# Kernel tuning notes

Hardware: AMD Instinct MI355X
Metric: run time of the kernel (lower is better)

The kernel has to match this reference:

```python
import jax, jax.numpy as jnp
import numpy as np

DIM = 4096
N_HEADS = 32
N_KV_HEADS = 8
HEAD_DIM = DIM // N_HEADS  # 128
B, S = 1, 2048
ROPE_THETA = 10000.0


def setup_inputs() -> dict:
    key = jax.random.key(0)
    kx, kq, kk, kv, ko = jax.random.split(key, 5)
    x = jax.random.normal(kx, (B, S, DIM), dtype=jnp.float32)
    # torch Linear weights are [out_features, in_features]
    wq = jax.random.normal(kq, (N_HEADS * HEAD_DIM, DIM), dtype=jnp.float32) * 0.02
    wk = jax.random.normal(kk, (N_KV_HEADS * HEAD_DIM, DIM), dtype=jnp.float32) * 0.02
    wv = jax.random.normal(kv, (N_KV_HEADS * HEAD_DIM, DIM), dtype=jnp.float32) * 0.02
    wo = jax.random.normal(ko, (DIM, N_HEADS * HEAD_DIM), dtype=jnp.float32) * 0.02
    # RoPE table [S, HEAD_DIM, 2]; frequencies repeated twice to match the
    # even/odd interleaved rotate_half convention of apply_rope.
    pos = jnp.arange(S, dtype=jnp.float32)
    inv_freq = 1.0 / (ROPE_THETA ** (jnp.arange(0, HEAD_DIM, 2, dtype=jnp.float32) / HEAD_DIM))
    ang = pos[:, None] * inv_freq[None, :]          # [S, HEAD_DIM/2]
    ang = jnp.repeat(ang, 2, axis=-1)               # [S, HEAD_DIM]
    rope_freqs = jnp.stack([jnp.cos(ang), jnp.sin(ang)], axis=-1)  # [S, HEAD_DIM, 2]
    return {"x": x, "wq": wq, "wk": wk, "wv": wv, "wo": wo,
            "rope_freqs": rope_freqs, "start_pos": 0}


def _rotate_half(t):
    # interleaved: (x0,x1,x2,x3,...) -> (-x1,x0,-x3,x2,...)
    t1 = t[..., ::2]
    t2 = t[..., 1::2]
    return jnp.stack((-t2, t1), axis=-1).reshape(t.shape)


def reference(x, wq, wk, wv, wo, rope_freqs, start_pos):
    b, s, _ = x.shape
    rep = N_HEADS // N_KV_HEADS
    scale = 1.0 / np.sqrt(HEAD_DIM)

    q = (x @ wq.T).reshape(b, s, N_HEADS, HEAD_DIM)
    k = (x @ wk.T).reshape(b, s, N_KV_HEADS, HEAD_DIM)
    v = (x @ wv.T).reshape(b, s, N_KV_HEADS, HEAD_DIM)

    cos = rope_freqs[..., 0][None, :, None, :]  # [1,S,1,HEAD_DIM]
    sin = rope_freqs[..., 1][None, :, None, :]
    q = q * cos + _rotate_half(q) * sin
    k = k * cos + _rotate_half(k) * sin

    # GQA without materializing repeated K/V: group query heads by kv head.
    qg = q.reshape(b, s, N_KV_HEADS, rep, HEAD_DIM)
    scores = jnp.einsum("bsgrd,btgd->bgrst", qg, k) * scale  # [B,KV,rep,S,S]
    causal = jnp.tril(jnp.ones((s, s), dtype=bool))
    scores = jnp.where(causal, scores, jnp.finfo(scores.dtype).min)
    attn = jax.nn.softmax(scores, axis=-1)
    out = jnp.einsum("bgrst,btgd->bsgrd", attn, v)           # [B,S,KV,rep,HEAD_DIM]
    out = out.reshape(b, s, N_HEADS * HEAD_DIM)
    return out @ wo.T
```

## Files before the change

### kernel.cpp

```cpp
#include <hip/hip_runtime.h>
#include <stdint.h>

#define DIM 4096
#define NH 32
#define NKV 8
#define HD 128
#define SEQ 2048
#define KVD 1024

typedef unsigned short u16;
typedef __attribute__((ext_vector_type(8))) short bf16x8;
typedef __attribute__((ext_vector_type(4))) float f32x4;

__device__ __forceinline__ float bf2f(u16 v){
  union { unsigned u; float f; } c; c.u = ((unsigned)v) << 16; return c.f;
}
__device__ __forceinline__ u16 f2bf(float f){
  union { float f; unsigned u; } c; c.f = f;
  unsigned u = c.u;
  u += 0x7FFF + ((u >> 16) & 1);
  return (u16)(u >> 16);
}
__device__ __forceinline__ unsigned pack2bf(float a, float b){
  return (unsigned)f2bf(a) | ((unsigned)f2bf(b) << 16);
}

__device__ __forceinline__ void gl_lds16(const void* g, void* l){
  __builtin_amdgcn_global_load_lds((const __attribute__((address_space(1))) void*)g,
                                   (__attribute__((address_space(3))) void*)l, 16, 0, 0);
}

#define VM0  asm volatile("s_waitcnt vmcnt(0)"  ::: "memory")
#define VM2  asm volatile("s_waitcnt vmcnt(2)"  ::: "memory")
#define VM4  asm volatile("s_waitcnt vmcnt(4)"  ::: "memory")
#define VM7  asm volatile("s_waitcnt vmcnt(7)"  ::: "memory")
#define VM10 asm volatile("s_waitcnt vmcnt(10)" ::: "memory")
#define LGKM0 asm volatile("s_waitcnt lgkmcnt(0)" ::: "memory")
#define SB0 __builtin_amdgcn_sched_barrier(0)
#define BAR __builtin_amdgcn_s_barrier()

__global__ void cvt_all(const float* __restrict__ x,  const float* __restrict__ wq,
                        const float* __restrict__ wk, const float* __restrict__ wv,
                        const float* __restrict__ wo,
                        u16* __restrict__ xb,  u16* __restrict__ wqb,
                        u16* __restrict__ wkb, u16* __restrict__ wvb,
                        u16* __restrict__ wob){
  const int b = blockIdx.x;
  const float* in; u16* out; int base;
  if      (b <  8192){ in = x;  out = xb;  base = b; }
  else if (b < 24576){ in = wq; out = wqb; base = b - 8192; }
  else if (b < 28672){ in = wk; out = wkb; base = b - 24576; }
  else if (b < 32768){ in = wv; out = wvb; base = b - 28672; }
  else               { in = wo; out = wob; base = b - 32768; }
  const int i = (base*256 + threadIdx.x)*4;
  float4 v = *(const float4*)(in + i);
  ushort4 o;
  o.x = f2bf(v.x); o.y = f2bf(v.y); o.z = f2bf(v.z); o.w = f2bf(v.w);
  *(ushort4*)(out + i) = o;
}

template<int BUNITS>
__global__ __launch_bounds__(512, 2) void gemmP(const u16* __restrict__ A,
    const u16* __restrict__ B, void* __restrict__ C0, void* __restrict__ C1,
    void* __restrict__ C2, const float* __restrict__ rf){
  constexpr int BN = BUNITS*64;
  __shared__ __align__(16) char lds[65536 + BUNITS*16384];
  const int t = threadIdx.x, w = t >> 6, l = t & 63;
  const int lg = l >> 4, li = l & 15;
  const int wr = w >> 2, wc = w & 3;
  const int idx = ((int)blockIdx.x & 7)*32 + ((int)blockIdx.x >> 3);
  const int bm = idx & 7, bn = idx >> 3;
  const int nt = 64, kbase = 0;
  const u16* Ab = A + (size_t)bm*256*DIM;
  const u16* Bb = B + (size_t)bn*BN*DIM;

  auto stA = [&](int k0, int abase, int u){
    const int r = u*64 + (t >> 3);
    gl_lds16(Ab + (size_t)r*DIM + k0 + (((t & 7) ^ (r & 7)) << 3),
             lds + abase + u*8192 + (t >> 3)*128 + (t & 7)*16);
  };
  auto stB = [&](int k0, int bbase, int u){
    const int r = u*64 + (t >> 3);
    gl_lds16(Bb + (size_t)r*DIM + k0 + (((t & 7) ^ (r & 7)) << 3),
             lds + bbase + u*8192 + (t >> 3)*128 + (t & 7)*16);
  };

  f32x4 acc[8][BUNITS] = {};
  bf16x8 bfr[BUNITS][2];

#define PH(p, ...) { \
    bf16x8 af[2][2]; \
    _Pragma("unroll") \
    for (int q = 0; q < 2; ++q){ \
      const int R = wr*128 + (2*(p)+q)*16 + li; \
      af[q][0] = *(const bf16x8*)(ldsA + R*128 + (( lg    ^ (R & 7)) << 4)); \
      af[q][1] = *(const bf16x8*)(ldsA + R*128 + (((lg+4) ^ (R & 7)) << 4)); \
    } \
    if ((p) == 0){ \
      _Pragma("unroll") \
      for (int j = 0; j < BUNITS; ++j){ \
        const int R = wc*(BUNITS*16) + j*16 + li; \
        bfr[j][0] = *(const bf16x8*)(ldsB + R*128 + (( lg    ^ (R & 7)) << 4)); \
        bfr[j][1] = *(const bf16x8*)(ldsB + R*128 + (((lg+4) ^ (R & 7)) << 4)); \
      } \
    } \
    __VA_ARGS__; \
    BAR; LGKM0; SB0; \
    __builtin_amdgcn_s_setprio(1); \
    _Pragma("unroll") \
    for (int q = 0; q < 2; ++q) \
      _Pragma("unroll") \
      for (int j = 0; j < BUNITS; ++j){ \
        acc[2*(p)+q][j] = __builtin_amdgcn_mfma_f32_16x16x32_bf16(af[q][0], bfr[j][0], acc[2*(p)+q][j], 0, 0, 0); \
        acc[2*(p)+q][j] = __builtin_amdgcn_mfma_f32_16x16x32_bf16(af[q][1], bfr[j][1], acc[2*(p)+q][j], 0, 0, 0); \
      } \
    __builtin_amdgcn_s_setprio(0); \
    BAR; }

  #pragma unroll
  for (int u = 0; u < BUNITS; ++u) stB(kbase, 65536, u);
  stA(kbase, 0, 0); stA(kbase, 0, 2);
  stA(kbase, 0, 1); stA(kbase, 0, 3);
  #pragma unroll
  for (int u = 0; u < BUNITS; ++u) stB(kbase + 64, 65536 + BUNITS*8192, u);
  stA(kbase + 64, 32768, 0); stA(kbase + 64, 32768, 2);
  VM7;
  BAR;

  for (int tt = 0; tt < nt; ++tt){
    const int k1 = kbase + (tt+1)*64, k2 = kbase + (tt+2)*64;
    const char* ldsA = lds + (tt & 1)*32768;
    const char* ldsB = lds + 65536 + (tt & 1)*BUNITS*8192;
    const int aCur = (tt & 1)*32768;
    const int aNxt = ((tt+1) & 1)*32768;
    const int bCur = 65536 + (tt & 1)*BUNITS*8192;

    PH(0, if (tt+1 < nt){ stA(k1, aNxt, 1); stA(k1, aNxt, 3); })
    PH(1, if (tt+2 < nt){ _Pragma("unroll")
                          for (int u = 0; u < BUNITS; ++u) stB(k2, bCur, u); }
          if (tt == nt-1){ VM0; }
          else if (tt == nt-2){ VM7; }
          else { VM10; } )
    PH(2, if (tt+2 < nt){ stA(k2, aCur, 0); stA(k2, aCur, 2); })
    PH(3, if (tt+1 < nt){
            if (tt+1 == nt-1){ VM2; }
            else { VM7; }
          } )
  }
#undef PH

  #pragma unroll
  for (int i = 0; i < 8; ++i){
    const int srow0 = bm*256 + wr*128 + i*16 + lg*4;
    #pragma unroll
    for (int j = 0; j < BUNITS; ++j){
      const int fc0 = bn*BN + wc*(BUNITS*16) + j*16;
      const int col = fc0 + li;
      if (fc0 < 5120){
        u16* C  = (fc0 < 4096) ? (u16*)C0 : (u16*)C1;
        const int ldc  = (fc0 < 4096) ? DIM : KVD;
        const int ccol = (fc0 < 4096) ? col : col - 4096;
        const int i4 = ((col & 127) >> 1) << 2;
        #pragma unroll
        for (int r = 0; r < 4; ++r){
          const float v = acc[i][j][r];
          const float p = __shfl_xor(v, 1);
          const int srow = srow0 + r;
          const float cs = rf[(size_t)srow*256 + i4];
          const float sn = rf[(size_t)srow*256 + i4 + 1];
          const float o = (col & 1) ? (v*cs + p*sn) : (v*cs - p*sn);
          C[(size_t)srow*ldc + ccol] = f2bf(o);
        }
      } else {
        u16* C = (u16*)C2;
        ushort4 o;
        o.x = f2bf(acc[i][j][0]); o.y = f2bf(acc[i][j][1]);
        o.z = f2bf(acc[i][j][2]); o.w = f2bf(acc[i][j][3]);
        *(ushort4*)&C[(size_t)(col - 5120)*SEQ + srow0] = o;
      }
    }
  }
}

__global__ __launch_bounds__(512, 1) void gemmO(const u16* __restrict__ A,
    const u16* __restrict__ B, float* __restrict__ C){
  __shared__ __align__(16) char lds[98304];
  const int t = threadIdx.x, w = t >> 6, l = t & 63;
  const int lg = l >> 4, li = l & 15;
  const int wr = w >> 2, wc = w & 3;
  const int idx = ((int)blockIdx.x & 7)*32 + ((int)blockIdx.x >> 3);
  const int bm = idx & 15, bn = idx >> 4;
  const int nt = 64;
  const u16* Ab = A + (size_t)bm*128*DIM;
  const u16* Bb = B + (size_t)bn*256*DIM;

  auto stA2 = [&](int k0, int slot){
    #pragma unroll
    for (int j = 0; j < 2; ++j){
      const int r = j*64 + (t >> 3);
      gl_lds16(Ab + (size_t)r*DIM + k0 + (((t & 7) ^ (r & 7)) << 3),
               lds + slot*16384 + r*128 + (t & 7)*16);
    }
  };
  auto stB1 = [&](int k0, int slot, int u){
    const int r = u*64 + (t >> 3);
    gl_lds16(Bb + (size_t)r*DIM + k0 + (((t & 7) ^ (r & 7)) << 3),
             lds + 32768 + slot*32768 + r*128 + (t & 7)*16);
  };

  f32x4 acc[4][4] = {};
  bf16x8 bfr[4][2];

#define PHO(p, ...) { \
    bf16x8 af[2][2]; \
    _Pragma("unroll") \
    for (int q = 0; q < 2; ++q){ \
      const int R = wr*64 + (2*(p)+q)*16 + li; \
      af[q][0] = *(const bf16x8*)(ldsA + R*128 + (( lg    ^ (R & 7)) << 4)); \
      af[q][1] = *(const bf16x8*)(ldsA + R*128 + (((lg+4) ^ (R & 7)) << 4)); \
    } \
    if ((p) == 0){ \
      _Pragma("unroll") \
      for (int j = 0; j < 4; ++j){ \
        const int R = wc*64 + j*16 + li; \
        bfr[j][0] = *(const bf16x8*)(ldsB + R*128 + (( lg    ^ (R & 7)) << 4)); \
        bfr[j][1] = *(const bf16x8*)(ldsB + R*128 + (((lg+4) ^ (R & 7)) << 4)); \
      } \
    } \
    __VA_ARGS__; \
    BAR; LGKM0; SB0; \
    __builtin_amdgcn_s_setprio(1); \
    _Pragma("unroll") \
    for (int q = 0; q < 2; ++q) \
      _Pragma("unroll") \
      for (int j = 0; j < 4; ++j){ \
        acc[2*(p)+q][j] = __builtin_amdgcn_mfma_f32_16x16x32_bf16(af[q][0], bfr[j][0], acc[2*(p)+q][j], 0, 0, 0); \
        acc[2*(p)+q][j] = __builtin_amdgcn_mfma_f32_16x16x32_bf16(af[q][1], bfr[j][1], acc[2*(p)+q][j], 0, 0, 0); \
      } \
    __builtin_amdgcn_s_setprio(0); \
    BAR; }

  #pragma unroll
  for (int u = 0; u < 4; ++u) stB1(0, 0, u);
  stA2(0, 0);
  #pragma unroll
  for (int u = 0; u < 4; ++u) stB1(64, 1, u);
  VM4; BAR;

  for (int tt = 0; tt < nt; ++tt){
    const char* ldsA = lds + (tt & 1)*16384;
    const char* ldsB = lds + 32768 + (tt & 1)*32768;
    const int k1 = (tt+1)*64, k2 = (tt+2)*64;

    PHO(0, if (tt+1 < nt){ stA2(k1, (tt+1) & 1); })
    PHO(1, if (tt+2 < nt){ stB1(k2, tt & 1, 0); stB1(k2, tt & 1, 1);
                           stB1(k2, tt & 1, 2); stB1(k2, tt & 1, 3); }
           if (tt+1 < nt){ if (tt+2 < nt){ VM4; } else { VM0; } } )
  }
#undef PHO

  #pragma unroll
  for (int i = 0; i < 4; ++i){
    const int srow = bm*128 + wr*64 + i*16 + lg*4;
    #pragma unroll
    for (int j = 0; j < 4; ++j){
      const int col = bn*256 + wc*64 + j*16 + li;
      #pragma unroll
      for (int r = 0; r < 4; ++r)
        C[(size_t)(srow + r)*DIM + col] = acc[i][j][r];
    }
  }
}

__global__ __launch_bounds__(256) void flash_attn(const u16* __restrict__ Q,
                                                  const u16* __restrict__ Kg,
                                                  const u16* __restrict__ Vt,
                                                  u16* __restrict__ O){
  __shared__ bf16x8 smK[2][64*16];
  __shared__ bf16x8 smV[2][128*8];
  __shared__ __align__(16) u16 smP[4][16*64];
  const int bid = blockIdx.x;
  const int h  = bid & 31;
  const int qt = 31 - (bid >> 5);
  const int g  = h >> 2;
  const int t = threadIdx.x, w = t >> 6, l = t & 63;
  const int lg = l >> 4, li = l & 15;

  bf16x8 qf[4];
  {
    const u16* qrow = Q + (size_t)(qt*64 + w*16 + li)*DIM + h*HD;
    #pragma unroll
    for (int kc = 0; kc < 4; ++kc)
      qf[kc] = *(const bf16x8*)(qrow + kc*32 + lg*8);
  }
  f32x4 accO[8] = {};
  float mrun = -1e30f, lsum = 0.f;
  const float SC = 0.08838834764831845f * 1.4426950408889634f;

  const int ksrow = t >> 4, ksslot = t & 15;
  const int vsrow = t >> 3, vsslot = t & 7;

  auto stage = [&](int kt, int b){
    #pragma unroll
    for (int j = 0; j < 4; ++j){
      const int krow = j*16 + ksrow;
      const int ksl = (ksslot & 8) | ((ksslot ^ (krow & 7)) & 7);
      gl_lds16(Kg + (size_t)(kt*64 + krow)*KVD + g*HD + ksl*8, (char*)&smK[b][0] + j*4096 + w*1024);
      const int vrow = j*32 + vsrow;
      const int vsl = (vsslot ^ (vrow & 7)) & 7;
      gl_lds16(Vt + (size_t)(g*HD + vrow)*SEQ + kt*64 + vsl*8, (char*)&smV[b][0] + j*4096 + w*1024);
    }
  };

  stage(0, 0);
  int buf = 0;
  u16* pw = &smP[w][0];

  for (int kt = 0; kt <= qt; ++kt){
    __syncthreads();
    if (kt < qt) stage(kt + 1, buf ^ 1);

    f32x4 sacc[4] = {};
    __builtin_amdgcn_s_setprio(1);
    #pragma unroll
    for (int kc = 0; kc < 4; ++kc){
      #pragma unroll
      for (int nj = 0; nj < 4; ++nj){
        const int R = nj*16 + li;
        int sl = lg + 4*kc;
        sl = (sl & 8) | ((sl ^ (R & 7)) & 7);
        sacc[nj] = __builtin_amdgcn_mfma_f32_16x16x32_bf16(smK[buf][R*16 + sl], qf[kc], sacc[nj], 0, 0, 0);
      }
    }
    __builtin_amdgcn_s_setprio(0);
    float p[4][4];
    #pragma unroll
    for (int nj = 0; nj < 4; ++nj)
      #pragma unroll
      for (int r = 0; r < 4; ++r)
        p[nj][r] = sacc[nj][r] * SC;
    if (kt == qt){
      const int qloc = w*16 + li;
      #pragma unroll
      for (int nj = 0; nj < 4; ++nj)
        #pragma unroll
        for (int r = 0; r < 4; ++r)
          if (nj*16 + lg*4 + r > qloc) p[nj][r] = -1e30f;
    }
    float mx = p[0][0];
    #pragma unroll
    for (int nj = 0; nj < 4; ++nj)
      #pragma unroll
      for (int r = 0; r < 4; ++r) mx = fmaxf(mx, p[nj][r]);
    mx = fmaxf(mx, __shfl_xor(mx, 16));
    mx = fmaxf(mx, __shfl_xor(mx, 32));
    if (!__all(mx - mrun <= 8.f)){
      const float mnew = fmaxf(mrun, mx);
      const float alpha = exp2f(mrun - mnew);
      lsum *= alpha;
      float al[4];
      #pragma unroll
      for (int r = 0; r < 4; ++r) al[r] = __shfl(alpha, (l & 48) | (lg*4 + r));
      #pragma unroll
      for (int dj = 0; dj < 8; ++dj)
        #pragma unroll
        for (int r = 0; r < 4; ++r) accO[dj][r] *= al[r];
      mrun = mnew;
    }
    float s = 0.f;
    #pragma unroll
    for (int nj = 0; nj < 4; ++nj)
      #pragma unroll
      for (int r = 0; r < 4; ++r){ p[nj][r] = exp2f(p[nj][r] - mrun); s += p[nj][r]; }
    s += __shfl_xor(s, 16);
    s += __shfl_xor(s, 32);
    lsum += s;
    #pragma unroll
    for (int nj = 0; nj < 4; ++nj){
      const int c = nj*2 + (lg >> 1);
      uint2 v; v.x = pack2bf(p[nj][0], p[nj][1]); v.y = pack2bf(p[nj][2], p[nj][3]);
      *(uint2*)((char*)pw + li*128 + ((c ^ (li & 7)) << 4) + ((lg & 1) << 3)) = v;
    }
    __builtin_amdgcn_s_setprio(1);
    #pragma unroll
    for (int kc2 = 0; kc2 < 2; ++kc2){
      const bf16x8 pf = *(const bf16x8*)((char*)pw + li*128 + (((kc2*4 + lg) ^ (li & 7)) << 4));
      #pragma unroll
      for (int dj = 0; dj < 8; ++dj){
        const int R = dj*16 + li;
        const bf16x8 vf = smV[buf][R*8 + ((lg + 4*kc2) ^ (R & 7))];
        accO[dj] = __builtin_amdgcn_mfma_f32_16x16x32_bf16(pf, vf, accO[dj], 0, 0, 0);
      }
    }
    __builtin_amdgcn_s_setprio(0);
    buf ^= 1;
  }
  float linv[4];
  #pragma unroll
  for (int r = 0; r < 4; ++r) linv[r] = 1.f / __shfl(lsum, (l & 48) | (lg*4 + r));
  #pragma unroll
  for (int dj = 0; dj < 8; ++dj)
    #pragma unroll
    for (int r = 0; r < 4; ++r)
      O[(size_t)(qt*64 + w*16 + lg*4 + r)*DIM + h*HD + dj*16 + li] = f2bf(accO[dj][r] * linv[r]);
}

extern "C" void kernel_launch(void* const* d_in, const int* in_sizes, int n_in,
                              void* d_out, int out_size, void* d_ws, size_t ws_size,
                              hipStream_t stream){
  const float* x  = (const float*)d_in[0];
  const float* wq = (const float*)d_in[1];
  const float* wk = (const float*)d_in[2];
  const float* wv = (const float*)d_in[3];
  const float* wo = (const float*)d_in[4];
  const float* rf = (const float*)d_in[5];
  float* out = (float*)d_out;

  char* ws = (char*)d_ws;
  size_t off = 0;
  auto alloc = [&](size_t nbytes){ void* p = ws + off; off += (nbytes + 255) & ~(size_t)255; return p; };
  u16* xb  = (u16*)alloc((size_t)SEQ*DIM*2);
  u16* wqb = (u16*)alloc((size_t)DIM*DIM*2);
  u16* wkb = (u16*)alloc((size_t)KVD*DIM*2);
  u16* wvb = (u16*)alloc((size_t)KVD*DIM*2);
  u16* wob = (u16*)alloc((size_t)DIM*DIM*2);
  u16* Qb  = (u16*)alloc((size_t)SEQ*DIM*2);
  u16* K8  = (u16*)alloc((size_t)SEQ*KVD*2);
  u16* Vtr = (u16*)alloc((size_t)KVD*SEQ*2);
  u16* AO  = (u16*)alloc((size_t)SEQ*DIM*2);

  cvt_all<<<49152, 256, 0, stream>>>(x, wq, wk, wv, wo, xb, wqb, wkb, wvb, wob);

  gemmP<3><<<256, 512, 0, stream>>>(xb, wqb, Qb, K8, Vtr, rf);

  flash_attn<<<SEQ/64 * NH, 256, 0, stream>>>(Qb, K8, Vtr, AO);

  gemmO<<<256, 512, 0, stream>>>(AO, wob, out);
}
```

Before: 296.3 us.

## Shrink QKV GEMM tile to 128x192 and double the grid with simpler pipeline

The fused QKV projection GEMM moves from 256x192 tiles on 256 blocks to 128x192 tiles on 512 blocks, using a two-phase double-buffered loop with reworked vmcnt waits. The goal is better CU occupancy and wave balance on a chip with many CUs, since 256 blocks leave part of the machine idle. In exchange each block does half the compute per B tile, so arithmetic intensity per LDS load drops and total global traffic for the weights rises.

```diff
diff --git a/kernel.cpp b/kernel.cpp
--- a/kernel.cpp
+++ b/kernel.cpp
@@ -31,10 +31,8 @@
 }
 
 #define VM0  asm volatile("s_waitcnt vmcnt(0)"  ::: "memory")
-#define VM2  asm volatile("s_waitcnt vmcnt(2)"  ::: "memory")
+#define VM3  asm volatile("s_waitcnt vmcnt(3)"  ::: "memory")
 #define VM4  asm volatile("s_waitcnt vmcnt(4)"  ::: "memory")
-#define VM7  asm volatile("s_waitcnt vmcnt(7)"  ::: "memory")
-#define VM10 asm volatile("s_waitcnt vmcnt(10)" ::: "memory")
 #define LGKM0 asm volatile("s_waitcnt lgkmcnt(0)" ::: "memory")
 #define SB0 __builtin_amdgcn_sched_barrier(0)
 #define BAR __builtin_amdgcn_s_barrier()
@@ -59,47 +57,48 @@
   *(ushort4*)(out + i) = o;
 }
 
-template<int BUNITS>
-__global__ __launch_bounds__(512, 2) void gemmP(const u16* __restrict__ A,
+__global__ __launch_bounds__(512, 2) void gemmQKV(const u16* __restrict__ A,
     const u16* __restrict__ B, void* __restrict__ C0, void* __restrict__ C1,
     void* __restrict__ C2, const float* __restrict__ rf){
-  constexpr int BN = BUNITS*64;
-  __shared__ __align__(16) char lds[65536 + BUNITS*16384];
+  __shared__ __align__(16) char lds[81920];
   const int t = threadIdx.x, w = t >> 6, l = t & 63;
   const int lg = l >> 4, li = l & 15;
   const int wr = w >> 2, wc = w & 3;
-  const int idx = ((int)blockIdx.x & 7)*32 + ((int)blockIdx.x >> 3);
-  const int bm = idx & 7, bn = idx >> 3;
-  const int nt = 64, kbase = 0;
-  const u16* Ab = A + (size_t)bm*256*DIM;
-  const u16* Bb = B + (size_t)bn*BN*DIM;
-
-  auto stA = [&](int k0, int abase, int u){
-    const int r = u*64 + (t >> 3);
-    gl_lds16(Ab + (size_t)r*DIM + k0 + (((t & 7) ^ (r & 7)) << 3),
-             lds + abase + u*8192 + (t >> 3)*128 + (t & 7)*16);
+  const int idx = ((int)blockIdx.x & 7)*64 + ((int)blockIdx.x >> 3);
+  const int bm = idx & 15, bn = idx >> 4;
+  const int nt = 64;
+  const u16* Ab = A + (size_t)bm*128*DIM;
+  const u16* Bb = B + (size_t)bn*192*DIM;
+
+  auto stA2 = [&](int k0, int slot){
+    #pragma unroll
+    for (int j = 0; j < 2; ++j){
+      const int r = j*64 + (t >> 3);
+      gl_lds16(Ab + (size_t)r*DIM + k0 + (((t & 7) ^ (r & 7)) << 3),
+               lds + slot*16384 + r*128 + (t & 7)*16);
+    }
   };
-  auto stB = [&](int k0, int bbase, int u){
+  auto stB1 = [&](int k0, int slot, int u){
     const int r = u*64 + (t >> 3);
     gl_lds16(Bb + (size_t)r*DIM + k0 + (((t & 7) ^ (r & 7)) << 3),
-             lds + bbase + u*8192 + (t >> 3)*128 + (t & 7)*16);
+             lds + 32768 + slot*24576 + r*128 + (t & 7)*16);
   };
 
-  f32x4 acc[8][BUNITS] = {};
-  bf16x8 bfr[BUNITS][2];
-
-#define PH(p, ...) { \
+  f32x4 acc[4][3] = {};
+  bf16x8 bfr[3][2];
+
+#define PHQ(p, ...) { \
     bf16x8 af[2][2]; \
     _Pragma("unroll") \
     for (int q = 0; q < 2; ++q){ \
-      const int R = wr*128 + (2*(p)+q)*16 + li; \
+      const int R = wr*64 + (2*(p)+q)*16 + li; \
       af[q][0] = *(const bf16x8*)(ldsA + R*128 + (( lg    ^ (R & 7)) << 4)); \
       af[q][1] = *(const bf16x8*)(ldsA + R*128 + (((lg+4) ^ (R & 7)) << 4)); \
     } \
     if ((p) == 0){ \
       _Pragma("unroll") \
-      for (int j = 0; j < BUNITS; ++j){ \
-        const int R = wc*(BUNITS*16) + j*16 + li; \
+      for (int j = 0; j < 3; ++j){ \
+        const int R = wc*48 + j*16 + li; \
         bfr[j][0] = *(const bf16x8*)(ldsB + R*128 + (( lg    ^ (R & 7)) << 4)); \
         bfr[j][1] = *(const bf16x8*)(ldsB + R*128 + (((lg+4) ^ (R & 7)) << 4)); \
       } \
@@ -110,7 +109,7 @@
     _Pragma("unroll") \
     for (int q = 0; q < 2; ++q) \
       _Pragma("unroll") \
-      for (int j = 0; j < BUNITS; ++j){ \
+      for (int j = 0; j < 3; ++j){ \
         acc[2*(p)+q][j] = __builtin_amdgcn_mfma_f32_16x16x32_bf16(af[q][0], bfr[j][0], acc[2*(p)+q][j], 0, 0, 0); \
         acc[2*(p)+q][j] = __builtin_amdgcn_mfma_f32_16x16x32_bf16(af[q][1], bfr[j][1], acc[2*(p)+q][j], 0, 0, 0); \
       } \
@@ -118,43 +117,29 @@
     BAR; }
 
   #pragma unroll
-  for (int u = 0; u < BUNITS; ++u) stB(kbase, 65536, u);
-  stA(kbase, 0, 0); stA(kbase, 0, 2);
-  stA(kbase, 0, 1); stA(kbase, 0, 3);
-  #pragma unroll
-  for (int u = 0; u < BUNITS; ++u) stB(kbase + 64, 65536 + BUNITS*8192, u);
-  stA(kbase + 64, 32768, 0); stA(kbase + 64, 32768, 2);
-  VM7;
-  BAR;
+  for (int u = 0; u < 3; ++u) stB1(0, 0, u);
+  stA2(0, 0);
+  #pragma unroll
+  for (int u = 0; u < 3; ++u) stB1(64, 1, u);
+  VM3; BAR;
 
   for (int tt = 0; tt < nt; ++tt){
-    const int k1 = kbase + (tt+1)*64, k2 = kbase + (tt+2)*64;
-    const char* ldsA = lds + (tt & 1)*32768;
-    const char* ldsB = lds + 65536 + (tt & 1)*BUNITS*8192;
-    const int aCur = (tt & 1)*32768;
-    const int aNxt = ((tt+1) & 1)*32768;
-    const int bCur = 65536 + (tt & 1)*BUNITS*8192;
-
-    PH(0, if (tt+1 < nt){ stA(k1, aNxt, 1); stA(k1, aNxt, 3); })
-    PH(1, if (tt+2 < nt){ _Pragma("unroll")
-                          for (int u = 0; u < BUNITS; ++u) stB(k2, bCur, u); }
-          if (tt == nt-1){ VM0; }
-          else if (tt == nt-2){ VM7; }
-          else { VM10; } )
-    PH(2, if (tt+2 < nt){ stA(k2, aCur, 0); stA(k2, aCur, 2); })
-    PH(3, if (tt+1 < nt){
-            if (tt+1 == nt-1){ VM2; }
-            else { VM7; }
-          } )
-  }
-#undef PH
-
-  #pragma unroll
-  for (int i = 0; i < 8; ++i){
-    const int srow0 = bm*256 + wr*128 + i*16 + lg*4;
-    #pragma unroll
-    for (int j = 0; j < BUNITS; ++j){
-      const int fc0 = bn*BN + wc*(BUNITS*16) + j*16;
+    const char* ldsA = lds + (tt & 1)*16384;
+    const char* ldsB = lds + 32768 + (tt & 1)*24576;
+    const int k1 = (tt+1)*64, k2 = (tt+2)*64;
+
+    PHQ(0, if (tt+1 < nt){ stA2(k1, (tt+1) & 1); })
+    PHQ(1, if (tt+2 < nt){ stB1(k2, tt & 1, 0); stB1(k2, tt & 1, 1); stB1(k2, tt & 1, 2); }
+           if (tt+1 < nt){ if (tt+2 < nt){ VM3; } else { VM0; } } )
+  }
+#undef PHQ
+
+  #pragma unroll
+  for (int i = 0; i < 4; ++i){
+    const int srow0 = bm*128 + wr*64 + i*16 + lg*4;
+    #pragma unroll
+    for (int j = 0; j < 3; ++j){
+      const int fc0 = bn*192 + wc*48 + j*16;
       const int col = fc0 + li;
       if (fc0 < 5120){
         u16* C  = (fc0 < 4096) ? (u16*)C0 : (u16*)C1;
@@ -431,7 +416,7 @@
 
   cvt_all<<<49152, 256, 0, stream>>>(x, wq, wk, wv, wo, xb, wqb, wkb, wvb, wob);
 
-  gemmP<3><<<256, 512, 0, stream>>>(xb, wqb, Qb, K8, Vtr, rf);
+  gemmQKV<<<512, 512, 0, stream>>>(xb, wqb, Qb, K8, Vtr, rf);
 
   flash_attn<<<SEQ/64 * NH, 256, 0, stream>>>(Qb, K8, Vtr, AO);
 
```

Result: slower. 305.9 us (+3.2%).
